# Kernel tuning notes

Measured on AMD Instinct MI355X. Metric: run time of the kernel, lower is better.

## Reference

```python
import jax, jax.numpy as jnp
import numpy as np
import math

D_MODEL = 1024
N_HEADS = 16
HEAD_DIM = D_MODEL // N_HEADS
BATCH = 2
SEQ = 4096


def setup_inputs() -> dict:
    key = jax.random.key(0)
    ks = jax.random.split(key, 12)
    s = 0.02
    inp = {
        "query": jax.random.normal(ks[0], (BATCH, SEQ, D_MODEL), jnp.float32),
        "key": jax.random.normal(ks[1], (BATCH, SEQ, D_MODEL), jnp.float32),
        "value": jax.random.normal(ks[2], (BATCH, SEQ, D_MODEL), jnp.float32),
        "mask": jnp.ones((1, 1, SEQ, SEQ), jnp.int32),
        "Wq": jax.random.normal(ks[3], (D_MODEL, D_MODEL), jnp.float32) * s,
        "bq": jax.random.normal(ks[4], (D_MODEL,), jnp.float32) * s,
        "Wk": jax.random.normal(ks[5], (D_MODEL, D_MODEL), jnp.float32) * s,
        "bk": jax.random.normal(ks[6], (D_MODEL,), jnp.float32) * s,
        "Wv": jax.random.normal(ks[7], (D_MODEL, D_MODEL), jnp.float32) * s,
        "bv": jax.random.normal(ks[8], (D_MODEL,), jnp.float32) * s,
        "Wo": jax.random.normal(ks[9], (D_MODEL, D_MODEL), jnp.float32) * s,
        "bo": jax.random.normal(ks[10], (D_MODEL,), jnp.float32) * s,
    }
    return inp


def reference(query, key, value, mask, Wq, bq, Wk, bk, Wv, bv, Wo, bo):
    B, S, D = query.shape
    scale = 1.0 / math.sqrt(HEAD_DIM)

    def proj_split(x, W, b):
        # Linear (torch convention x @ W.T + b) then split heads -> [B, H, S, Dh]
        y = x @ W.T + b
        return y.reshape(B, -1, N_HEADS, HEAD_DIM).transpose(0, 2, 1, 3)

    q = proj_split(query, Wq, bq)
    k = proj_split(key, Wk, bk)
    v = proj_split(value, Wv, bv)

    # naive materialized scores [B, H, Sq, Sk]
    scores = jnp.einsum("bhqd,bhkd->bhqk", q, k) * scale
    scores = jnp.where(mask == 0, jnp.float32(-1e9), scores)
    probs = jax.nn.softmax(scores, axis=-1)
    attn = jnp.einsum("bhqk,bhkd->bhqd", probs, v)

    # combine heads -> [B, S, D]
    out = attn.transpose(0, 2, 1, 3).reshape(B, S, D)
    return out @ Wo.T + bo
```

## Files before the change

### kernel.cpp

```cpp
#include <hip/hip_runtime.h>

typedef float f32x4  __attribute__((ext_vector_type(4)));
typedef float f32x16 __attribute__((ext_vector_type(16)));
typedef __bf16 bf16x8 __attribute__((ext_vector_type(8)));
typedef unsigned u32x2 __attribute__((ext_vector_type(2)));
typedef unsigned u32x4 __attribute__((ext_vector_type(4)));

#define DEV static __device__ __forceinline__

constexpr int SEQ_ = 4096;
constexpr int DM_  = 1024;
constexpr int NH_  = 16;
constexpr int DH_  = 64;

DEV unsigned short f2bf(float f) {
    union { float f; unsigned u; } v; v.f = f;
    return (unsigned short)((v.u + 0x7fffu + ((v.u >> 16) & 1u)) >> 16);
}

DEV unsigned cvtpk_bf16(float lo, float hi) {
    unsigned r;
    asm("v_cvt_pk_bf16_f32 %0, %1, %2" : "=v"(r) : "v"(lo), "v"(hi));
    return r;
}

DEV void gll16(const void* g, void* l) {
    __builtin_amdgcn_global_load_lds(
        (const __attribute__((address_space(1))) void*)g,
        (__attribute__((address_space(3))) void*)l,
        16, 0, 0);
}

__global__ void cast_all(const float* __restrict__ q, const float* __restrict__ k,
                         const float* __restrict__ v, const float* __restrict__ wq,
                         const float* __restrict__ wk, const float* __restrict__ wv,
                         const float* __restrict__ wo, unsigned short* __restrict__ dst)
{
    constexpr int NA = 2 * SEQ_ * DM_ / 4;
    constexpr int NW = DM_ * DM_ / 4;
    int i = blockIdx.x * blockDim.x + threadIdx.x;
    if (i >= 3 * NA + 4 * NW) return;
    const float4* s4;
    if (i < NA)            s4 = (const float4*)q + i;
    else if (i < 2 * NA)   s4 = (const float4*)k + (i - NA);
    else if (i < 3 * NA)   s4 = (const float4*)v + (i - 2 * NA);
    else {
        int j = i - 3 * NA;
        int t = j >> 18;
        int l = j & (NW - 1);
        s4 = (const float4*)(t == 0 ? wq : t == 1 ? wk : t == 2 ? wv : wo) + l;
    }
    float4 val = *s4;
    ushort4 o;
    o.x = f2bf(val.x); o.y = f2bf(val.y); o.z = f2bf(val.z); o.w = f2bf(val.w);
    ((ushort4*)dst)[i] = o;
}

template<int MODE>
__global__ __launch_bounds__(256, 2)
void gemm_bt(const unsigned short* __restrict__ A,
             const unsigned short* __restrict__ Bw,
             const float* __restrict__ bias,
             void* __restrict__ Cout,
             int M, int N, int K, float oscale)
{
    __shared__ char As[128 * 128];
    __shared__ char Bs[128 * 128];

    const int tid = threadIdx.x;
    const int w = tid >> 6, lane = tid & 63;
    const int wr = w >> 1, wc = w & 1;
    const int lr = lane & 15, lg = lane >> 4;

    const int nwg = gridDim.x * gridDim.y;
    const int bid = blockIdx.y * gridDim.x + blockIdx.x;
    const int id  = (bid & 7) * (nwg >> 3) + (bid >> 3);
    const int bx = id & 7;
    const int by = id >> 3;
    const int m0 = by * 128, n0 = bx * 128;

    f32x4 acc[4][4] = {};

    for (int kt = 0; kt < K / 64; ++kt) {
        const int k0 = kt * 64;
        __syncthreads();
        #pragma unroll
        for (int i = 0; i < 4; ++i) {
            int ch = w * 4 + i;
            int o = (ch * 64 + lane) * 16;
            int row = o >> 7, cb = o & 127;
            int cbs = cb ^ ((row & 7) << 4);
            gll16((const char*)A  + ((size_t)(m0 + row) * K + k0) * 2 + cbs, As + ch * 1024);
            gll16((const char*)Bw + ((size_t)(n0 + row) * K + k0) * 2 + cbs, Bs + ch * 1024);
        }
        __syncthreads();

        #pragma unroll
        for (int kf = 0; kf < 2; ++kf) {
            bf16x8 af[4], bfv[4];
            #pragma unroll
            for (int mf = 0; mf < 4; ++mf) {
                int row = wr * 64 + mf * 16 + lr;
                int cb = (kf * 64 + lg * 16) ^ ((row & 7) << 4);
                af[mf] = *(const bf16x8*)(As + row * 128 + cb);
            }
            #pragma unroll
            for (int nf = 0; nf < 4; ++nf) {
                int row = wc * 64 + nf * 16 + lr;
                int cb = (kf * 64 + lg * 16) ^ ((row & 7) << 4);
                bfv[nf] = *(const bf16x8*)(Bs + row * 128 + cb);
            }
            #pragma unroll
            for (int mf = 0; mf < 4; ++mf)
                #pragma unroll
                for (int nf = 0; nf < 4; ++nf)
                    acc[mf][nf] = __builtin_amdgcn_mfma_f32_16x16x32_bf16(
                        af[mf], bfv[nf], acc[mf][nf], 0, 0, 0);
        }
    }

    #pragma unroll
    for (int nf = 0; nf < 4; ++nf) {
        int gn = n0 + wc * 64 + nf * 16 + lr;
        float bv = bias[gn];
        #pragma unroll
        for (int mf = 0; mf < 4; ++mf) {
            #pragma unroll
            for (int r = 0; r < 4; ++r) {
                int gm = m0 + wr * 64 + mf * 16 + lg * 4 + r;
                float val = (acc[mf][nf][r] + bv) * oscale;
                if (MODE == 1) {
                    ((float*)Cout)[(size_t)gm * N + gn] = val;
                } else {
                    int b = gm >> 12, s = gm & (SEQ_ - 1);
                    int h = gn >> 6, dh = gn & (DH_ - 1);
                    size_t idx = (MODE == 0)
                        ? (((size_t)(b * NH_ + h) * SEQ_ + s) * DH_ + dh)
                        : (((size_t)(b * NH_ + h) * DH_ + dh) * SEQ_ + s);
                    ((unsigned short*)Cout)[idx] = f2bf(val);
                }
            }
        }
    }
}

__global__ __launch_bounds__(512, 4)
void attn_fwd(const unsigned short* __restrict__ Qb,
              const unsigned short* __restrict__ Kb,
              const unsigned short* __restrict__ Vtb,
              unsigned short* __restrict__ ctx)
{
    __shared__ char Ks[2][64 * 128];
    __shared__ char Vs[2][64 * 128];

    const int tid = threadIdx.x;
    const int w = tid >> 6, lane = tid & 63;
    const int l31 = lane & 31, hi = lane >> 5;

    const int nwg = gridDim.x * gridDim.y;
    const int bid = blockIdx.y * gridDim.x + blockIdx.x;
    const int id  = (bid & 7) * (nwg >> 3) + (bid >> 3);
    const int qt = id & 15;
    const int bh = id >> 4;

    const unsigned short* Qh = Qb + (size_t)bh * SEQ_ * DH_;
    const int q0 = qt * 256 + w * 32;
    const int q  = q0 + l31;

    bf16x8 qa[4];
    #pragma unroll
    for (int kk = 0; kk < 4; ++kk)
        qa[kk] = *(const bf16x8*)(Qh + (size_t)q * DH_ + kk * 16 + hi * 8);

    const int so = (w * 64 + lane) * 16;
    const int srow = so >> 7, scb = so & 127;
    const int scbs = scb ^ ((srow & 7) << 4);
    const char* kgl = (const char*)(Kb  + (size_t)bh * SEQ_ * DH_) + (size_t)srow * DH_ * 2 + scbs;
    const char* vgl = (const char*)(Vtb + (size_t)bh * DH_ * SEQ_) + (size_t)srow * SEQ_ * 2 + scbs;
    char* k0d = Ks[0] + w * 1024; char* v0d = Vs[0] + w * 1024;
    char* k1d = Ks[1] + w * 1024; char* v1d = Vs[1] + w * 1024;

    unsigned ldoff[2][4];
    #pragma unroll
    for (int sub = 0; sub < 2; ++sub)
        #pragma unroll
        for (int kk = 0; kk < 4; ++kk) {
            int row = sub * 32 + l31;
            ldoff[sub][kk] = row * 128 + ((32 * kk + 16 * hi) ^ ((row & 7) << 4));
        }

    float lsum = 0.f;
    f32x16 o_acc[2] = {};

    auto stage = [&](char* kdst, char* vdst, int t) {
        gll16(kgl + (size_t)t * (64 * DH_ * 2), kdst);
        gll16(vgl + (size_t)t * (64 * 2),       vdst);
    };

    auto compute = [&](const char* Ksb, const char* Vsb) {
        f32x16 sacc[2] = {};
        __builtin_amdgcn_s_setprio(1);
        #pragma unroll
        for (int kk = 0; kk < 4; ++kk) {
            #pragma unroll
            for (int sub = 0; sub < 2; ++sub) {
                bf16x8 kf = *(const bf16x8*)(Ksb + ldoff[sub][kk]);
                sacc[sub] = __builtin_amdgcn_mfma_f32_32x32x16_bf16(kf, qa[kk], sacc[sub], 0, 0, 0);
            }
        }
        __builtin_amdgcn_s_setprio(0);

        unsigned c0[8], c1[8];
        #pragma unroll
        for (int g = 0; g < 8; ++g) {
            int sub = g >> 2, u = g & 3;
            float e0 = __builtin_amdgcn_exp2f(sacc[sub][4 * u + 0]);
            float e1 = __builtin_amdgcn_exp2f(sacc[sub][4 * u + 1]);
            float e2 = __builtin_amdgcn_exp2f(sacc[sub][4 * u + 2]);
            float e3 = __builtin_amdgcn_exp2f(sacc[sub][4 * u + 3]);
            lsum += (e0 + e1) + (e2 + e3);
            c0[g] = cvtpk_bf16(e0, e1);
            c1[g] = cvtpk_bf16(e2, e3);
        }

        __builtin_amdgcn_s_setprio(1);
        #pragma unroll
        for (int ks = 0; ks < 4; ++ks) {
            u32x2 s0 = __builtin_amdgcn_permlane32_swap(c0[2 * ks], c0[2 * ks + 1], false, false);
            u32x2 s1 = __builtin_amdgcn_permlane32_swap(c1[2 * ks], c1[2 * ks + 1], false, false);
            u32x4 pw; pw[0] = s0[0]; pw[1] = s1[0]; pw[2] = s0[1]; pw[3] = s1[1];
            bf16x8 pfrag = __builtin_bit_cast(bf16x8, pw);
            #pragma unroll
            for (int dsub = 0; dsub < 2; ++dsub) {
                bf16x8 vf = *(const bf16x8*)(Vsb + ldoff[dsub][ks]);
                o_acc[dsub] = __builtin_amdgcn_mfma_f32_32x32x16_bf16(vf, pfrag, o_acc[dsub], 0, 0, 0);
            }
        }
        __builtin_amdgcn_s_setprio(0);
    };

    stage(k0d, v0d, 0);
    for (int kt = 0; kt < SEQ_ / 64; kt += 2) {
        __syncthreads();
        stage(k1d, v1d, kt + 1);
        compute(Ks[0], Vs[0]);
        __syncthreads();
        if (kt + 2 < SEQ_ / 64) stage(k0d, v0d, kt + 2);
        compute(Ks[1], Vs[1]);
    }

    const int b = bh >> 4, h = bh & 15;
    const float lt = lsum + __shfl_xor(lsum, 32);
    const float inv = 1.f / lt;
    unsigned short* orow = ctx + ((size_t)(b * SEQ_ + q)) * DM_ + h * 64;
    #pragma unroll
    for (int dsub = 0; dsub < 2; ++dsub)
        #pragma unroll
        for (int u = 0; u < 4; ++u) {
            ushort4 o4;
            o4.x = f2bf(o_acc[dsub][4 * u + 0] * inv);
            o4.y = f2bf(o_acc[dsub][4 * u + 1] * inv);
            o4.z = f2bf(o_acc[dsub][4 * u + 2] * inv);
            o4.w = f2bf(o_acc[dsub][4 * u + 3] * inv);
            *(ushort4*)(orow + dsub * 32 + 8 * u + 4 * hi) = o4;
        }
}

extern "C" void kernel_launch(void* const* d_in, const int* in_sizes, int n_in,
                              void* d_out, int out_size, void* d_ws, size_t ws_size,
                              hipStream_t stream)
{
    const float* q_in = (const float*)d_in[0];
    const float* k_in = (const float*)d_in[1];
    const float* v_in = (const float*)d_in[2];
    const float* Wq = (const float*)d_in[4];
    const float* bq = (const float*)d_in[5];
    const float* Wk = (const float*)d_in[6];
    const float* bk = (const float*)d_in[7];
    const float* Wv = (const float*)d_in[8];
    const float* bv = (const float*)d_in[9];
    const float* Wo = (const float*)d_in[10];
    const float* bo = (const float*)d_in[11];

    char* ws = (char*)d_ws;
    const size_t MB16 = (size_t)2 * SEQ_ * DM_ * 2;
    const size_t WSZ  = (size_t)DM_ * DM_ * 2;

    unsigned short* Xq  = (unsigned short*)(ws);
    unsigned short* Xk  = (unsigned short*)(ws + MB16);
    unsigned short* Xv  = (unsigned short*)(ws + 2 * MB16);
    unsigned short* Wqb = (unsigned short*)(ws + 3 * MB16);
    unsigned short* Wkb = (unsigned short*)(ws + 3 * MB16 + WSZ);
    unsigned short* Wvb = (unsigned short*)(ws + 3 * MB16 + 2 * WSZ);
    unsigned short* Wob = (unsigned short*)(ws + 3 * MB16 + 3 * WSZ);
    unsigned short* Qb  = (unsigned short*)(ws + 3 * MB16 + 4 * WSZ);
    unsigned short* Kb  = (unsigned short*)(ws + 4 * MB16 + 4 * WSZ);
    unsigned short* Vt  = (unsigned short*)(ws + 5 * MB16 + 4 * WSZ);
    unsigned short* Ctx = Xq;

    constexpr int NTOT4 = (3 * 2 * SEQ_ * DM_ + 4 * DM_ * DM_) / 4;
    cast_all<<<(NTOT4 + 255) / 256, 256, 0, stream>>>(q_in, k_in, v_in, Wq, Wk, Wv, Wo,
                                                      (unsigned short*)ws);

    const float qscale = 0.125f * 1.44269504088896340736f;
    dim3 gg(DM_ / 128, 2 * SEQ_ / 128);
    gemm_bt<0><<<gg, 256, 0, stream>>>(Xq, Wqb, bq, Qb, 2 * SEQ_, DM_, DM_, qscale);
    gemm_bt<0><<<gg, 256, 0, stream>>>(Xk, Wkb, bk, Kb, 2 * SEQ_, DM_, DM_, 1.0f);
    gemm_bt<2><<<gg, 256, 0, stream>>>(Xv, Wvb, bv, Vt, 2 * SEQ_, DM_, DM_, 1.0f);

    attn_fwd<<<dim3(16, 32), 512, 0, stream>>>(Qb, Kb, Vt, Ctx);

    gemm_bt<1><<<gg, 256, 0, stream>>>(Ctx, Wob, bo, d_out, 2 * SEQ_, DM_, DM_, 1.0f);
}
```

Before: 258.9 us.

## Merge QKV GEMMs into one launch and deepen attention K/V prefetch to four stages

The three Q/K/V projection GEMMs are folded into a single launch using blockIdx.z to pick the projection. This removes two kernel launches and lets the three GEMMs' tail waves overlap. The attention kernel moves from double buffering with two barriers per pair of tiles to a 4-buffer ring that prefetches three tiles ahead, with explicit vmcnt waits and one barrier per tile. This doubles LDS use to 64KB per block, which may cut occupancy below the declared 4 blocks per CU.

```diff
diff --git a/kernel.cpp b/kernel.cpp
--- a/kernel.cpp
+++ b/kernel.cpp
@@ -57,16 +57,10 @@
 }
 
 template<int MODE>
-__global__ __launch_bounds__(256, 2)
-void gemm_bt(const unsigned short* __restrict__ A,
-             const unsigned short* __restrict__ Bw,
-             const float* __restrict__ bias,
-             void* __restrict__ Cout,
-             int M, int N, int K, float oscale)
-{
-    __shared__ char As[128 * 128];
-    __shared__ char Bs[128 * 128];
-
+DEV void gemm_body(const unsigned short* A, const unsigned short* Bw,
+                   const float* bias, void* Cout, int M, int N, int K,
+                   float oscale, char* As, char* Bs)
+{
     const int tid = threadIdx.x;
     const int w = tid >> 6, lane = tid & 63;
     const int wr = w >> 1, wc = w & 1;
@@ -144,14 +138,43 @@
     }
 }
 
+__global__ __launch_bounds__(256, 2)
+void gemm_qkv(const unsigned short* __restrict__ Xq, const unsigned short* __restrict__ Xk,
+              const unsigned short* __restrict__ Xv, const unsigned short* __restrict__ Wqb,
+              const unsigned short* __restrict__ Wkb, const unsigned short* __restrict__ Wvb,
+              const float* __restrict__ bq, const float* __restrict__ bk,
+              const float* __restrict__ bv_, unsigned short* __restrict__ Qb,
+              unsigned short* __restrict__ Kb, unsigned short* __restrict__ Vt,
+              float qscale)
+{
+    __shared__ char As[128 * 128];
+    __shared__ char Bs[128 * 128];
+    const int z = blockIdx.z;
+    if (z == 0)
+        gemm_body<0>(Xq, Wqb, bq, Qb, 2 * SEQ_, DM_, DM_, qscale, As, Bs);
+    else if (z == 1)
+        gemm_body<0>(Xk, Wkb, bk, Kb, 2 * SEQ_, DM_, DM_, 1.0f, As, Bs);
+    else
+        gemm_body<2>(Xv, Wvb, bv_, Vt, 2 * SEQ_, DM_, DM_, 1.0f, As, Bs);
+}
+
+__global__ __launch_bounds__(256, 2)
+void gemm_out(const unsigned short* __restrict__ A, const unsigned short* __restrict__ Bw,
+              const float* __restrict__ bias, float* __restrict__ Cout)
+{
+    __shared__ char As[128 * 128];
+    __shared__ char Bs[128 * 128];
+    gemm_body<1>(A, Bw, bias, Cout, 2 * SEQ_, DM_, DM_, 1.0f, As, Bs);
+}
+
 __global__ __launch_bounds__(512, 4)
 void attn_fwd(const unsigned short* __restrict__ Qb,
               const unsigned short* __restrict__ Kb,
               const unsigned short* __restrict__ Vtb,
               unsigned short* __restrict__ ctx)
 {
-    __shared__ char Ks[2][64 * 128];
-    __shared__ char Vs[2][64 * 128];
+    __shared__ char Ks[4][64 * 128];
+    __shared__ char Vs[4][64 * 128];
 
     const int tid = threadIdx.x;
     const int w = tid >> 6, lane = tid & 63;
@@ -177,8 +200,6 @@
     const int scbs = scb ^ ((srow & 7) << 4);
     const char* kgl = (const char*)(Kb  + (size_t)bh * SEQ_ * DH_) + (size_t)srow * DH_ * 2 + scbs;
     const char* vgl = (const char*)(Vtb + (size_t)bh * DH_ * SEQ_) + (size_t)srow * SEQ_ * 2 + scbs;
-    char* k0d = Ks[0] + w * 1024; char* v0d = Vs[0] + w * 1024;
-    char* k1d = Ks[1] + w * 1024; char* v1d = Vs[1] + w * 1024;
 
     unsigned ldoff[2][4];
     #pragma unroll
@@ -192,9 +213,9 @@
     float lsum = 0.f;
     f32x16 o_acc[2] = {};
 
-    auto stage = [&](char* kdst, char* vdst, int t) {
-        gll16(kgl + (size_t)t * (64 * DH_ * 2), kdst);
-        gll16(vgl + (size_t)t * (64 * 2),       vdst);
+    auto stage = [&](int buf, int t) {
+        gll16(kgl + (size_t)t * (64 * DH_ * 2), Ks[buf] + w * 1024);
+        gll16(vgl + (size_t)t * (64 * 2),       Vs[buf] + w * 1024);
     };
 
     auto compute = [&](const char* Ksb, const char* Vsb) {
@@ -239,15 +260,27 @@
         __builtin_amdgcn_s_setprio(0);
     };
 
-    stage(k0d, v0d, 0);
-    for (int kt = 0; kt < SEQ_ / 64; kt += 2) {
-        __syncthreads();
-        stage(k1d, v1d, kt + 1);
-        compute(Ks[0], Vs[0]);
-        __syncthreads();
-        if (kt + 2 < SEQ_ / 64) stage(k0d, v0d, kt + 2);
-        compute(Ks[1], Vs[1]);
+    stage(0, 0); stage(1, 1); stage(2, 2);
+
+    for (int t = 0; t < 61; ++t) {
+        asm volatile("s_waitcnt vmcnt(4)" ::: "memory");
+        __builtin_amdgcn_s_barrier();
+        __builtin_amdgcn_sched_barrier(0);
+        stage((t + 3) & 3, t + 3);
+        compute(Ks[t & 3], Vs[t & 3]);
     }
+    asm volatile("s_waitcnt vmcnt(4)" ::: "memory");
+    __builtin_amdgcn_s_barrier();
+    __builtin_amdgcn_sched_barrier(0);
+    compute(Ks[1], Vs[1]);
+    asm volatile("s_waitcnt vmcnt(2)" ::: "memory");
+    __builtin_amdgcn_s_barrier();
+    __builtin_amdgcn_sched_barrier(0);
+    compute(Ks[2], Vs[2]);
+    asm volatile("s_waitcnt vmcnt(0)" ::: "memory");
+    __builtin_amdgcn_s_barrier();
+    __builtin_amdgcn_sched_barrier(0);
+    compute(Ks[3], Vs[3]);
 
     const int b = bh >> 4, h = bh & 15;
     const float lt = lsum + __shfl_xor(lsum, 32);
@@ -303,12 +336,11 @@
                                                       (unsigned short*)ws);
 
     const float qscale = 0.125f * 1.44269504088896340736f;
-    dim3 gg(DM_ / 128, 2 * SEQ_ / 128);
-    gemm_bt<0><<<gg, 256, 0, stream>>>(Xq, Wqb, bq, Qb, 2 * SEQ_, DM_, DM_, qscale);
-    gemm_bt<0><<<gg, 256, 0, stream>>>(Xk, Wkb, bk, Kb, 2 * SEQ_, DM_, DM_, 1.0f);
-    gemm_bt<2><<<gg, 256, 0, stream>>>(Xv, Wvb, bv, Vt, 2 * SEQ_, DM_, DM_, 1.0f);
+    dim3 gg3(DM_ / 128, 2 * SEQ_ / 128, 3);
+    gemm_qkv<<<gg3, 256, 0, stream>>>(Xq, Xk, Xv, Wqb, Wkb, Wvb, bq, bk, bv,
+                                      Qb, Kb, Vt, qscale);
 
     attn_fwd<<<dim3(16, 32), 512, 0, stream>>>(Qb, Kb, Vt, Ctx);
 
-    gemm_bt<1><<<gg, 256, 0, stream>>>(Ctx, Wob, bo, d_out, 2 * SEQ_, DM_, DM_, 1.0f);
-}
+    gemm_out<<<dim3(DM_ / 128, 2 * SEQ_ / 128), 256, 0, stream>>>(Ctx, Wob, bo, (float*)d_out);
+}
```

New measurement: 263.7 us. About the same (+1.8%).
